# Kernel tuning notes

Measured on AMD Instinct MI355X. Metric: run time of the kernel, lower is better.

## Reference

```python
import jax, jax.numpy as jnp
import numpy as np
from jax.scipy.linalg import solve_triangular

CHUNK = 32


def _l2norm(x):
    return x / jnp.sqrt(jnp.sum(x * x, axis=-1, keepdims=True))


def setup_inputs() -> dict:
    key = jax.random.key(0)
    kq, kk, kv, kb = jax.random.split(key, 4)
    b, h, L, d = 2, 8, 4096, 128
    q = jax.random.normal(kq, (b, h, L, d), dtype=jnp.float32)
    k = jax.random.normal(kk, (b, h, L, d), dtype=jnp.float32)
    v = jax.random.normal(kv, (b, h, L, d), dtype=jnp.float32)
    beta = jax.random.uniform(kb, (b, h, L), dtype=jnp.float32)
    return {"q": q, "k": k, "v": v, "beta": beta}


def _delta_rule_chunkwise(q, k, v, beta, chunk_size=CHUNK):
    b, h, L, d_k = q.shape
    d_v = v.shape[-1]
    pad_len = (-L) % chunk_size
    if pad_len:
        q = jnp.pad(q, ((0, 0), (0, 0), (0, pad_len), (0, 0)))
        k = jnp.pad(k, ((0, 0), (0, 0), (0, pad_len), (0, 0)))
        v = jnp.pad(v, ((0, 0), (0, 0), (0, pad_len), (0, 0)))
        beta = jnp.pad(beta, ((0, 0), (0, 0), (0, pad_len)))
    L_pad = L + pad_len
    n = L_pad // chunk_size
    c = chunk_size

    q = _l2norm(q)
    k = _l2norm(k)
    v = v * beta[..., None]
    k_beta = k * beta[..., None]

    # -> [b, h, n, c, d]
    qc = q.reshape(b, h, n, c, d_k)
    kc = k.reshape(b, h, n, c, d_k)
    vc = v.reshape(b, h, n, c, d_v)
    kbc = k_beta.reshape(b, h, n, c, d_k)

    # Intra-chunk UT transform: inv = (I + strictly_lower(k_beta @ k^T))^{-1}
    # (equivalent to the sequential forward-substitution loop in the torch code)
    A = jnp.einsum('bhnce,bhnfe->bhncf', kbc, kc)          # [b,h,n,c,c]
    strict_lower = jnp.tril(jnp.ones((c, c), dtype=A.dtype), k=-1)
    T = A * strict_lower + jnp.eye(c, dtype=A.dtype)        # unit lower-triangular
    eye_b = jnp.broadcast_to(jnp.eye(c, dtype=A.dtype), T.shape)
    inv = solve_triangular(T, eye_b, lower=True)            # [b,h,n,c,c]

    u = jnp.einsum('bhncf,bhnfd->bhncd', inv, vc)           # [b,h,n,c,d_v]
    w = jnp.einsum('bhncf,bhnfk->bhnck', inv, kbc)          # [b,h,n,c,d_k]

    # Cross-chunk recurrence over n chunks (sequential in n)
    causal = jnp.tril(jnp.ones((c, c), dtype=q.dtype))      # incl. diagonal
    qs = jnp.moveaxis(qc, 2, 0)   # [n,b,h,c,d_k]
    ks = jnp.moveaxis(kc, 2, 0)
    us = jnp.moveaxis(u, 2, 0)
    ws = jnp.moveaxis(w, 2, 0)

    S0 = jnp.zeros((b, h, d_k, d_v), dtype=q.dtype)

    def step(S, xs):
        q_i, k_i, u_i, w_i = xs
        local_attn = jnp.einsum('bhce,bhfe->bhcf', q_i, k_i) * causal
        u_adj = u_i - jnp.einsum('bhck,bhkd->bhcd', w_i, S)
        o_i = jnp.einsum('bhck,bhkd->bhcd', q_i, S) \
            + jnp.einsum('bhcf,bhfd->bhcd', local_attn, u_adj)
        S_new = S + jnp.einsum('bhck,bhcd->bhkd', k_i, u_adj)
        return S_new, o_i

    S_final, outs = jax.lax.scan(step, S0, (qs, ks, us, ws))
    out = jnp.moveaxis(outs, 0, 2).reshape(b, h, L_pad, d_v)
    if pad_len:
        out = out[:, :, :L]
    return out, S_final


def reference(q, k, v, beta):
    return _delta_rule_chunkwise(q, k, v, beta)
```

## Files before the change

kernel.cpp:

```cpp
#include <hip/hip_runtime.h>


#define Bb 2
#define Hh 8
#define Ll 4096
#define Dd 128
#define DP (Dd + 4)
#define Cc 32
#define CP2 33
#define NC (Ll / Cc)
#define BHn (Bb * Hh)

#define SLAB 30720

typedef float  f32x16 __attribute__((ext_vector_type(16)));
typedef short  bf16x8 __attribute__((ext_vector_type(8)));

#define WAITVM(N) asm volatile("s_waitcnt vmcnt(" #N ")" ::: "memory")

__device__ __forceinline__ short f2bf(float x) {
    union { float f; unsigned u; } a; a.f = x;
    const unsigned r = a.u + 0x7FFFu + ((a.u >> 16) & 1u);
    return (short)(r >> 16);
}

__device__ __forceinline__ float bf2f(short h) {
    union { unsigned u; float f; } t;
    t.u = ((unsigned)(unsigned short)h) << 16;
    return t.f;
}

__device__ __forceinline__ unsigned cvt_pk_bf16(float lo, float hi) {
    unsigned r;
    asm("v_cvt_pk_bf16_f32 %0, %1, %2" : "=v"(r) : "v"(lo), "v"(hi));
    return r;
}

__device__ __forceinline__ bf16x8 mk_bop(const f32x16& T, int m) {
    const int o = 8 * m;
    const unsigned a01 = cvt_pk_bf16(T[o + 0], T[o + 1]);
    const unsigned a23 = cvt_pk_bf16(T[o + 2], T[o + 3]);
    const unsigned b01 = cvt_pk_bf16(T[o + 4], T[o + 5]);
    const unsigned b23 = cvt_pk_bf16(T[o + 6], T[o + 7]);
    const auto r0 = __builtin_amdgcn_permlane32_swap(a01, b01, false, false);
    const auto r1 = __builtin_amdgcn_permlane32_swap(a23, b23, false, false);
    union { unsigned u[4]; bf16x8 v; } out;
    out.u[0] = r0[0]; out.u[1] = r1[0]; out.u[2] = r0[1]; out.u[3] = r1[1];
    return out.v;
}

__device__ __forceinline__ void gl_lds16(const void* gsrc, void* ldst) {
    __builtin_amdgcn_global_load_lds(
        (const __attribute__((address_space(1))) unsigned int*)gsrc,
        (__attribute__((address_space(3))) unsigned int*)ldst, 16, 0, 0);
}

__device__ __forceinline__ void split8(const float4& a, const float4& b,
                                       bf16x8& hi, bf16x8& lo) {
    const float x[8] = {a.x, a.y, a.z, a.w, b.x, b.y, b.z, b.w};
    #pragma unroll
    for (int j = 0; j < 8; ++j) {
        const short hs = f2bf(x[j]);
        hi[j] = hs;
        lo[j] = f2bf(x[j] - bf2f(hs));
    }
}

__device__ __forceinline__ void fma4(float4& acc, float s, const float4& x) {
    acc.x += s * x.x; acc.y += s * x.y; acc.z += s * x.z; acc.w += s * x.w;
}

template <bool QNB>
__global__ __launch_bounds__(256, 4) void prep_kernel(
    const float* __restrict__ q, const float* __restrict__ k,
    const float* __restrict__ v, const float* __restrict__ beta,
    float* __restrict__ wsU, float* __restrict__ wsNq,
    short* __restrict__ wsWb, short* __restrict__ wsKtb,
    short* __restrict__ wsAttnb, short* __restrict__ wsQnb)
{
    __shared__ float sK[Cc][DP];
    __shared__ float sA[Cc][CP2];
    __shared__ float sInv[Cc][CP2];
    __shared__ float sBeta[Cc], sNk[Cc], sNq[Cc];

    const int tid = threadIdx.x;
    const int blk = blockIdx.x;
    const int bh = blk / NC;
    const int ch = blk % NC;
    const size_t base = (size_t)(bh * Ll + ch * Cc) * Dd;

    for (int e = tid; e < Cc * Dd / 4; e += 256) {
        const int r = e >> 5, c4 = e & 31;
        ((float4*)&sK[r][0])[c4] = ((const float4*)(k + base))[e];
    }
    if (tid < Cc) sBeta[tid] = beta[bh * Ll + ch * Cc + tid];
    __syncthreads();

    {
        const int row = tid >> 2, part = tid & 3;
        float s = 0.f;
        if (row < Cc) {
            const float4* src = (const float4*)&sK[row][0];
            #pragma unroll
            for (int j = 0; j < 8; ++j) {
                const float4 t = src[part + j * 4];
                s += t.x * t.x + t.y * t.y + t.z * t.z + t.w * t.w;
            }
        } else {
            const float4* src =
                (const float4*)(q + base + (size_t)(row - Cc) * Dd);
            #pragma unroll
            for (int j = 0; j < 8; ++j) {
                const float4 t = src[part + j * 4];
                s += t.x * t.x + t.y * t.y + t.z * t.z + t.w * t.w;
            }
        }
        s += __shfl_xor(s, 1);
        s += __shfl_xor(s, 2);
        if (part == 0) {
            const float r = 1.0f / sqrtf(s);
            if (row < Cc) sNk[row] = r; else sNq[row - Cc] = r;
        }
    }
    __syncthreads();

    if (tid < Cc) wsNq[bh * Ll + ch * Cc + tid] = sNq[tid];

    for (int e = tid; e < Cc * Dd / 4; e += 256) {
        const int r = e >> 5, c4 = e & 31;
        float4 kk = ((float4*)&sK[r][0])[c4];
        const float nk = sNk[r];
        kk.x *= nk; kk.y *= nk; kk.z *= nk; kk.w *= nk;
        ((float4*)&sK[r][0])[c4] = kk;
    }
    __syncthreads();

    const int wid = tid >> 6;
    const int lc = tid & 31;
    const int lh = (tid >> 5) & 1;
    const size_t cbase = (size_t)blk * Cc * Dd;
    const size_t abase = (size_t)blk * Cc * Cc;

    if (wid == 0) {
        f32x16 D, D2;
        #pragma unroll
        for (int r = 0; r < 16; ++r) { D[r] = 0.f; D2[r] = 0.f; }
        #pragma unroll
        for (int ks = 0; ks < 8; ++ks) {
            const float4 a = ((const float4*)&sK[lc][0])[4 * ks + 2 * lh];
            const float4 b = ((const float4*)&sK[lc][0])[4 * ks + 2 * lh + 1];
            bf16x8 hi, lo;
            split8(a, b, hi, lo);
            D  = __builtin_amdgcn_mfma_f32_32x32x16_bf16(hi, hi, D,  0, 0, 0);
            D2 = __builtin_amdgcn_mfma_f32_32x32x16_bf16(hi, lo, D2, 0, 0, 0);
            D2 = __builtin_amdgcn_mfma_f32_32x32x16_bf16(lo, hi, D2, 0, 0, 0);
        }
        #pragma unroll
        for (int r = 0; r < 16; ++r) {
            const int row = (r & 3) + 8 * (r >> 2) + 4 * lh;
            sA[row][lc] = (D[r] + D2[r]) * sBeta[row];
        }
        asm volatile("s_waitcnt lgkmcnt(0)" ::: "memory");
        __builtin_amdgcn_sched_barrier(0);

        float inv[Cc];
        #pragma unroll
        for (int m = 0; m < Cc; ++m) inv[m] = (m == lc) ? 1.f : 0.f;
        #pragma unroll
        for (int i = 1; i < Cc; ++i) {
            float s = 0.f;
            #pragma unroll
            for (int m = 0; m < i; ++m) s += sA[i][m] * inv[m];
            inv[i] = (lc == i) ? 1.f : -s;
        }
        if (lh == 0) {
            #pragma unroll
            for (int m = 0; m < Cc; ++m) sInv[m][lc] = inv[m];
        }
    } else if (wid == 1) {
        const float nq = sNq[lc];
        const float* qrow = q + base + (size_t)lc * Dd;
        f32x16 D, D2;
        #pragma unroll
        for (int r = 0; r < 16; ++r) { D[r] = 0.f; D2[r] = 0.f; }
        #pragma unroll
        for (int ks = 0; ks < 8; ++ks) {
            float4 a = ((const float4*)qrow)[4 * ks + 2 * lh];
            float4 b = ((const float4*)qrow)[4 * ks + 2 * lh + 1];
            a.x *= nq; a.y *= nq; a.z *= nq; a.w *= nq;
            b.x *= nq; b.y *= nq; b.z *= nq; b.w *= nq;
            bf16x8 hiQ, loQ;
            split8(a, b, hiQ, loQ);
            if constexpr (QNB) {
                ((bf16x8*)(wsQnb + cbase))[(2 * ks + lh) * 32 + lc] = hiQ;
            }
            const float4 ka = ((const float4*)&sK[lc][0])[4 * ks + 2 * lh];
            const float4 kb2 = ((const float4*)&sK[lc][0])[4 * ks + 2 * lh + 1];
            bf16x8 hiK, loK;
            split8(ka, kb2, hiK, loK);
            D  = __builtin_amdgcn_mfma_f32_32x32x16_bf16(hiQ, hiK, D,  0, 0, 0);
            D2 = __builtin_amdgcn_mfma_f32_32x32x16_bf16(hiQ, loK, D2, 0, 0, 0);
            D2 = __builtin_amdgcn_mfma_f32_32x32x16_bf16(loQ, hiK, D2, 0, 0, 0);
        }
        #pragma unroll
        for (int r = 0; r < 16; ++r) {
            const int row = (r & 3) + 8 * (r >> 2) + 4 * lh;
            const float val = (lc <= row) ? (D[r] + D2[r]) : 0.f;
            wsAttnb[abase + ((lc >> 3) << 8) + (row << 3) + (lc & 7)] =
                f2bf(val);
        }
    } else {
        const int t = tid - 128;
        #pragma unroll
        for (int it = 0; it < 4; ++it) {
            const int g = t + it * 128;
            const int B = g >> 5, ddl = g & 31;
            const int dd = ((B >> 2) << 5) + ddl;
            const int cc0 = (B & 3) << 3;
            bf16x8 pk;
            #pragma unroll
            for (int j = 0; j < 8; ++j) pk[j] = f2bf(sK[cc0 + j][dd]);
            ((bf16x8*)(wsKtb + cbase))[g] = pk;
        }
    }
    __syncthreads();

    {
        const int c = tid >> 3, g = tid & 7, dd0 = g * 16;
        float4 u0{}, u1{}, u2{}, u3{}, w0{}, w1{}, w2{}, w3{};
        for (int f = 0; f <= c; ++f) {
            const float ivb = sInv[c][f] * sBeta[f];
            const float4* vr = (const float4*)(v + base + (size_t)f * Dd + dd0);
            const float4* kr = (const float4*)&sK[f][dd0];
            fma4(u0, ivb, vr[0]); fma4(u1, ivb, vr[1]);
            fma4(u2, ivb, vr[2]); fma4(u3, ivb, vr[3]);
            fma4(w0, ivb, kr[0]); fma4(w1, ivb, kr[1]);
            fma4(w2, ivb, kr[2]); fma4(w3, ivb, kr[3]);
        }
        const int rh = (c & 3) + ((c >> 3) << 2) + (((c >> 2) & 1) << 4);
        const float uu[16] = {u0.x, u0.y, u0.z, u0.w, u1.x, u1.y, u1.z, u1.w,
                              u2.x, u2.y, u2.z, u2.w, u3.x, u3.y, u3.z, u3.w};
        #pragma unroll
        for (int j = 0; j < 16; ++j) {
            const int dd = dd0 + j;
            wsU[cbase + ((dd >> 5) << 10) + (rh << 5) + (dd & 31)] = uu[j];
        }
        bf16x8 p0, p1;
        p0[0] = f2bf(-w0.x); p0[1] = f2bf(-w0.y); p0[2] = f2bf(-w0.z);
        p0[3] = f2bf(-w0.w); p0[4] = f2bf(-w1.x); p0[5] = f2bf(-w1.y);
        p0[6] = f2bf(-w1.z); p0[7] = f2bf(-w1.w);
        p1[0] = f2bf(-w2.x); p1[1] = f2bf(-w2.y); p1[2] = f2bf(-w2.z);
        p1[3] = f2bf(-w2.w); p1[4] = f2bf(-w3.x); p1[5] = f2bf(-w3.y);
        p1[6] = f2bf(-w3.z); p1[7] = f2bf(-w3.w);
        ((bf16x8*)(wsWb + cbase))[(2 * g) * 32 + c] = p0;
        ((bf16x8*)(wsWb + cbase))[(2 * g + 1) * 32 + c] = p1;
    }
}

template <bool QNB>
__device__ __forceinline__ void stage_slab(
    char* slab, int bh, int ch, int colBase, int lane,
    const short* __restrict__ wsWb, const short* __restrict__ wsKtb,
    const short* __restrict__ wsQnb, const short* __restrict__ wsAttnb,
    const float* __restrict__ wsU)
{
    const size_t cb = (size_t)(bh * NC + ch) * (Cc * Dd);
    const size_t ab = (size_t)(bh * NC + ch) * (Cc * Cc);
    const char* srcW = (const char*)(wsWb + cb);
    const char* srcK = (const char*)(wsKtb + cb);
    const char* srcA = (const char*)(wsAttnb + ab);
    const int l16 = lane * 16;
    #pragma unroll
    for (int g = 0; g < 8; ++g)
        gl_lds16(srcW + g * 1024 + l16, slab + g * 1024);
    #pragma unroll
    for (int g = 0; g < 8; ++g)
        gl_lds16(srcK + g * 1024 + l16, slab + 8192 + g * 1024);
    if constexpr (QNB) {
        const char* srcQ = (const char*)(wsQnb + cb);
        #pragma unroll
        for (int g = 0; g < 8; ++g)
            gl_lds16(srcQ + g * 1024 + l16, slab + 16384 + g * 1024);
    }
    #pragma unroll
    for (int g = 0; g < 2; ++g)
        gl_lds16(srcA + g * 1024 + l16, slab + 24576 + g * 1024);
    const float* srcU = wsU + cb + (colBase << 5);
    #pragma unroll
    for (int g = 0; g < 4; ++g)
        gl_lds16(srcU + g * 256 + lane * 4, slab + 26624 + g * 1024);
}

template <bool QNB>
__device__ __forceinline__ void compute_chunk(
    const char* slab, int bh, int ch, int colBase, int c, int h,
    const float* __restrict__ q, const float* __restrict__ wsNq,
    f32x16& S0, f32x16& S1, f32x16& S2, f32x16& S3, float* __restrict__ out)
{
    const bf16x8* Wf = (const bf16x8*)slab;
    const bf16x8* Kf = (const bf16x8*)(slab + 8192);
    const bf16x8* Qf = (const bf16x8*)(slab + 16384);
    const bf16x8* Af = (const bf16x8*)(slab + 24576);
    const float*  Uf = (const float*)(slab + 26624);

    bf16x8 qa[8];
    if constexpr (QNB) {
        #pragma unroll
        for (int ks = 0; ks < 8; ++ks) qa[ks] = Qf[(2 * ks + h) * 32 + c];
    } else {
        const size_t qb = (size_t)(bh * Ll + ch * Cc) * Dd;
        const float rq = wsNq[bh * Ll + ch * Cc + c];
        #pragma unroll
        for (int ks = 0; ks < 8; ++ks) {
            const float4 a = ((const float4*)(q + qb))[c * 32 + 4 * ks + 2 * h];
            const float4 b = ((const float4*)(q + qb))[c * 32 + 4 * ks + 2 * h + 1];
            union { unsigned u[4]; bf16x8 v; } t;
            t.u[0] = cvt_pk_bf16(a.x * rq, a.y * rq);
            t.u[1] = cvt_pk_bf16(a.z * rq, a.w * rq);
            t.u[2] = cvt_pk_bf16(b.x * rq, b.y * rq);
            t.u[3] = cvt_pk_bf16(b.z * rq, b.w * rq);
            qa[ks] = t.v;
        }
    }

    f32x16 Ua, Ub, O1, O2;
    #pragma unroll
    for (int r = 0; r < 16; ++r) {
        Ua[r] = Uf[(r + 16 * h) * 32 + c];
        Ub[r] = 0.f; O1[r] = 0.f; O2[r] = 0.f;
    }

    #pragma unroll
    for (int ks = 0; ks < 8; ++ks) {
        const f32x16& T = (ks < 2) ? S0 : (ks < 4) ? S1 : (ks < 6) ? S2 : S3;
        const bf16x8 sB = mk_bop(T, ks & 1);
        const bf16x8 wA = Wf[(2 * ks + h) * 32 + c];
        if (ks < 4)
            Ua = __builtin_amdgcn_mfma_f32_32x32x16_bf16(wA, sB, Ua, 0, 0, 0);
        else
            Ub = __builtin_amdgcn_mfma_f32_32x32x16_bf16(wA, sB, Ub, 0, 0, 0);
        if (ks & 1)
            O2 = __builtin_amdgcn_mfma_f32_32x32x16_bf16(qa[ks], sB, O2, 0, 0, 0);
        else
            O1 = __builtin_amdgcn_mfma_f32_32x32x16_bf16(qa[ks], sB, O1, 0, 0, 0);
    }

    f32x16 Us;
    #pragma unroll
    for (int r = 0; r < 16; ++r) Us[r] = Ua[r] + Ub[r];

    const bf16x8 uB0 = mk_bop(Us, 0);
    const bf16x8 uB1 = mk_bop(Us, 1);

    S0 = __builtin_amdgcn_mfma_f32_32x32x16_bf16(Kf[(0 + h) * 32 + c],  uB0, S0, 0, 0, 0);
    S0 = __builtin_amdgcn_mfma_f32_32x32x16_bf16(Kf[(2 + h) * 32 + c],  uB1, S0, 0, 0, 0);
    S1 = __builtin_amdgcn_mfma_f32_32x32x16_bf16(Kf[(4 + h) * 32 + c],  uB0, S1, 0, 0, 0);
    S1 = __builtin_amdgcn_mfma_f32_32x32x16_bf16(Kf[(6 + h) * 32 + c],  uB1, S1, 0, 0, 0);
    S2 = __builtin_amdgcn_mfma_f32_32x32x16_bf16(Kf[(8 + h) * 32 + c],  uB0, S2, 0, 0, 0);
    S2 = __builtin_amdgcn_mfma_f32_32x32x16_bf16(Kf[(10 + h) * 32 + c], uB1, S2, 0, 0, 0);
    S3 = __builtin_amdgcn_mfma_f32_32x32x16_bf16(Kf[(12 + h) * 32 + c], uB0, S3, 0, 0, 0);
    S3 = __builtin_amdgcn_mfma_f32_32x32x16_bf16(Kf[(14 + h) * 32 + c], uB1, S3, 0, 0, 0);

    O1 = __builtin_amdgcn_mfma_f32_32x32x16_bf16(Af[(0 + h) * 32 + c], uB0, O1, 0, 0, 0);
    O2 = __builtin_amdgcn_mfma_f32_32x32x16_bf16(Af[(2 + h) * 32 + c], uB1, O2, 0, 0, 0);

    const size_t qb = (size_t)(bh * Ll + ch * Cc) * Dd;
    #pragma unroll
    for (int r = 0; r < 16; ++r) {
        const int row = (r & 3) + 8 * (r >> 2) + 4 * h;
        out[qb + (size_t)row * Dd + colBase + c] = O1[r] + O2[r];
    }
}

template <bool QNB>
__device__ __forceinline__ void pcstep(
    int ch, char* cur, char* nxt, bool dostage, int wid,
    int bh, int colBase, int c, int h, int lane,
    const float* __restrict__ q, const float* __restrict__ wsNq,
    const short* __restrict__ wsWb, const short* __restrict__ wsKtb,
    const short* __restrict__ wsAttnb, const short* __restrict__ wsQnb,
    const float* __restrict__ wsU,
    f32x16& S0, f32x16& S1, f32x16& S2, f32x16& S3, float* __restrict__ out)
{
    if (wid == 0) {
        compute_chunk<QNB>(cur, bh, ch, colBase, c, h, q, wsNq,
                           S0, S1, S2, S3, out);
    } else {
        if (dostage) {
            stage_slab<QNB>(nxt, bh, ch + 2, colBase, lane,
                            wsWb, wsKtb, wsQnb, wsAttnb, wsU);
            if constexpr (QNB) WAITVM(30); else WAITVM(22);
        } else {
            WAITVM(0);
        }
    }
    __builtin_amdgcn_s_barrier();
}

template <bool QNB>
__global__ __launch_bounds__(128, 1) void scan_kernel(
    const float* __restrict__ q, const float* __restrict__ wsU,
    const short* __restrict__ wsWb, const short* __restrict__ wsKtb,
    const short* __restrict__ wsAttnb, const short* __restrict__ wsQnb,
    const float* __restrict__ wsNq, float* __restrict__ out)
{
    __shared__ __attribute__((aligned(16))) char sl0[SLAB];
    __shared__ __attribute__((aligned(16))) char sl1[SLAB];
    __shared__ __attribute__((aligned(16))) char sl2[SLAB];

    const int tid = threadIdx.x;
    const int wid = tid >> 6;
    const int lane = tid & 63;
    const int h = lane >> 5;
    const int c = lane & 31;
    const int bh = blockIdx.x;
    const int colBase = blockIdx.y * 32;

    f32x16 S0, S1, S2, S3;
    #pragma unroll
    for (int r = 0; r < 16; ++r) { S0[r]=0.f; S1[r]=0.f; S2[r]=0.f; S3[r]=0.f; }

    if (wid == 1) {
        stage_slab<QNB>(sl0, bh, 0, colBase, lane, wsWb, wsKtb, wsQnb,
                        wsAttnb, wsU);
        stage_slab<QNB>(sl1, bh, 1, colBase, lane, wsWb, wsKtb, wsQnb,
                        wsAttnb, wsU);
        if constexpr (QNB) WAITVM(30); else WAITVM(22);
    }
    __builtin_amdgcn_s_barrier();

    #pragma unroll 1
    for (int it = 0; it < 42; ++it) {
        const int ch = it * 3;
        pcstep<QNB>(ch + 0, sl0, sl2, true, wid, bh, colBase, c, h, lane,
                    q, wsNq, wsWb, wsKtb, wsAttnb, wsQnb, wsU,
                    S0, S1, S2, S3, out);
        pcstep<QNB>(ch + 1, sl1, sl0, true, wid, bh, colBase, c, h, lane,
                    q, wsNq, wsWb, wsKtb, wsAttnb, wsQnb, wsU,
                    S0, S1, S2, S3, out);
        pcstep<QNB>(ch + 2, sl2, sl1, true, wid, bh, colBase, c, h, lane,
                    q, wsNq, wsWb, wsKtb, wsAttnb, wsQnb, wsU,
                    S0, S1, S2, S3, out);
    }
    pcstep<QNB>(126, sl0, sl2, false, wid, bh, colBase, c, h, lane,
                q, wsNq, wsWb, wsKtb, wsAttnb, wsQnb, wsU, S0, S1, S2, S3, out);
    pcstep<QNB>(127, sl1, sl0, false, wid, bh, colBase, c, h, lane,
                q, wsNq, wsWb, wsKtb, wsAttnb, wsQnb, wsU, S0, S1, S2, S3, out);

    if (wid == 0) {
        const size_t soff = (size_t)Bb * Hh * Ll * Dd;
        #pragma unroll
        for (int t = 0; t < 4; ++t) {
            const f32x16& T = (t == 0) ? S0 : (t == 1) ? S1 : (t == 2) ? S2 : S3;
            #pragma unroll
            for (int r = 0; r < 16; ++r) {
                const int row = 32 * t + (r & 3) + 8 * (r >> 2) + 4 * h;
                out[soff + (size_t)bh * Dd * Dd + (size_t)row * Dd + colBase + c]
                    = T[r];
            }
        }
    }
}

extern "C" void kernel_launch(void* const* d_in, const int* in_sizes, int n_in,
                              void* d_out, int out_size, void* d_ws,
                              size_t ws_size, hipStream_t stream) {
    const float* q    = (const float*)d_in[0];
    const float* k    = (const float*)d_in[1];
    const float* v    = (const float*)d_in[2];
    const float* beta = (const float*)d_in[3];
    float* out = (float*)d_out;

    const size_t nQK = (size_t)BHn * Ll * Dd;
    float* wsU    = (float*)d_ws;
    float* wsNq   = wsU + nQK;
    short* wsWb   = (short*)(wsNq + (size_t)BHn * Ll);
    short* wsKtb  = wsWb + nQK;
    short* wsAttnb = wsKtb + nQK;
    short* wsQnb  = wsAttnb + (size_t)BHn * NC * Cc * Cc;
    const size_t need_qnb = (size_t)((char*)(wsQnb + nQK) - (char*)d_ws);

    if (ws_size >= need_qnb) {
        prep_kernel<true><<<dim3(BHn * NC), 256, 0, stream>>>(
            q, k, v, beta, wsU, wsNq, wsWb, wsKtb, wsAttnb, wsQnb);
        scan_kernel<true><<<dim3(BHn, 4), 128, 0, stream>>>(
            q, wsU, wsWb, wsKtb, wsAttnb, wsQnb, wsNq, out);
    } else {
        prep_kernel<false><<<dim3(BHn * NC), 256, 0, stream>>>(
            q, k, v, beta, wsU, wsNq, wsWb, wsKtb, wsAttnb, wsQnb);
        scan_kernel<false><<<dim3(BHn, 4), 128, 0, stream>>>(
            q, wsU, wsWb, wsKtb, wsAttnb, wsQnb, wsNq, out);
    }
}
```

Before: 316.5 us.

## Split per-chunk scan compute across two waves with LDS exchange of partials

The sequential scan step was done by a single compute wave while a second wave staged the next slabs. Now two compute waves each handle half of the K dimension of the state (S0/S1 versus S2/S3). They exchange partial U and O sums through small LDS buffers with an extra barrier per chunk, and a third wave takes over staging. The goal is to shorten the serial MFMA dependency chain per chunk. The cost is an additional barrier per chunk and LDS traffic on the critical path.

```diff
diff --git a/kernel.cpp b/kernel.cpp
--- a/kernel.cpp
+++ b/kernel.cpp
@@ -17,6 +17,7 @@
 typedef short  bf16x8 __attribute__((ext_vector_type(8)));
 
 #define WAITVM(N) asm volatile("s_waitcnt vmcnt(" #N ")" ::: "memory")
+#define WAITLGKM0 asm volatile("s_waitcnt lgkmcnt(0)" ::: "memory")
 
 __device__ __forceinline__ short f2bf(float x) {
     union { float f; unsigned u; } a; a.f = x;
@@ -292,87 +293,6 @@
 }
 
 template <bool QNB>
-__device__ __forceinline__ void compute_chunk(
-    const char* slab, int bh, int ch, int colBase, int c, int h,
-    const float* __restrict__ q, const float* __restrict__ wsNq,
-    f32x16& S0, f32x16& S1, f32x16& S2, f32x16& S3, float* __restrict__ out)
-{
-    const bf16x8* Wf = (const bf16x8*)slab;
-    const bf16x8* Kf = (const bf16x8*)(slab + 8192);
-    const bf16x8* Qf = (const bf16x8*)(slab + 16384);
-    const bf16x8* Af = (const bf16x8*)(slab + 24576);
-    const float*  Uf = (const float*)(slab + 26624);
-
-    bf16x8 qa[8];
-    if constexpr (QNB) {
-        #pragma unroll
-        for (int ks = 0; ks < 8; ++ks) qa[ks] = Qf[(2 * ks + h) * 32 + c];
-    } else {
-        const size_t qb = (size_t)(bh * Ll + ch * Cc) * Dd;
-        const float rq = wsNq[bh * Ll + ch * Cc + c];
-        #pragma unroll
-        for (int ks = 0; ks < 8; ++ks) {
-            const float4 a = ((const float4*)(q + qb))[c * 32 + 4 * ks + 2 * h];
-            const float4 b = ((const float4*)(q + qb))[c * 32 + 4 * ks + 2 * h + 1];
-            union { unsigned u[4]; bf16x8 v; } t;
-            t.u[0] = cvt_pk_bf16(a.x * rq, a.y * rq);
-            t.u[1] = cvt_pk_bf16(a.z * rq, a.w * rq);
-            t.u[2] = cvt_pk_bf16(b.x * rq, b.y * rq);
-            t.u[3] = cvt_pk_bf16(b.z * rq, b.w * rq);
-            qa[ks] = t.v;
-        }
-    }
-
-    f32x16 Ua, Ub, O1, O2;
-    #pragma unroll
-    for (int r = 0; r < 16; ++r) {
-        Ua[r] = Uf[(r + 16 * h) * 32 + c];
-        Ub[r] = 0.f; O1[r] = 0.f; O2[r] = 0.f;
-    }
-
-    #pragma unroll
-    for (int ks = 0; ks < 8; ++ks) {
-        const f32x16& T = (ks < 2) ? S0 : (ks < 4) ? S1 : (ks < 6) ? S2 : S3;
-        const bf16x8 sB = mk_bop(T, ks & 1);
-        const bf16x8 wA = Wf[(2 * ks + h) * 32 + c];
-        if (ks < 4)
-            Ua = __builtin_amdgcn_mfma_f32_32x32x16_bf16(wA, sB, Ua, 0, 0, 0);
-        else
-            Ub = __builtin_amdgcn_mfma_f32_32x32x16_bf16(wA, sB, Ub, 0, 0, 0);
-        if (ks & 1)
-            O2 = __builtin_amdgcn_mfma_f32_32x32x16_bf16(qa[ks], sB, O2, 0, 0, 0);
-        else
-            O1 = __builtin_amdgcn_mfma_f32_32x32x16_bf16(qa[ks], sB, O1, 0, 0, 0);
-    }
-
-    f32x16 Us;
-    #pragma unroll
-    for (int r = 0; r < 16; ++r) Us[r] = Ua[r] + Ub[r];
-
-    const bf16x8 uB0 = mk_bop(Us, 0);
-    const bf16x8 uB1 = mk_bop(Us, 1);
-
-    S0 = __builtin_amdgcn_mfma_f32_32x32x16_bf16(Kf[(0 + h) * 32 + c],  uB0, S0, 0, 0, 0);
-    S0 = __builtin_amdgcn_mfma_f32_32x32x16_bf16(Kf[(2 + h) * 32 + c],  uB1, S0, 0, 0, 0);
-    S1 = __builtin_amdgcn_mfma_f32_32x32x16_bf16(Kf[(4 + h) * 32 + c],  uB0, S1, 0, 0, 0);
-    S1 = __builtin_amdgcn_mfma_f32_32x32x16_bf16(Kf[(6 + h) * 32 + c],  uB1, S1, 0, 0, 0);
-    S2 = __builtin_amdgcn_mfma_f32_32x32x16_bf16(Kf[(8 + h) * 32 + c],  uB0, S2, 0, 0, 0);
-    S2 = __builtin_amdgcn_mfma_f32_32x32x16_bf16(Kf[(10 + h) * 32 + c], uB1, S2, 0, 0, 0);
-    S3 = __builtin_amdgcn_mfma_f32_32x32x16_bf16(Kf[(12 + h) * 32 + c], uB0, S3, 0, 0, 0);
-    S3 = __builtin_amdgcn_mfma_f32_32x32x16_bf16(Kf[(14 + h) * 32 + c], uB1, S3, 0, 0, 0);
-
-    O1 = __builtin_amdgcn_mfma_f32_32x32x16_bf16(Af[(0 + h) * 32 + c], uB0, O1, 0, 0, 0);
-    O2 = __builtin_amdgcn_mfma_f32_32x32x16_bf16(Af[(2 + h) * 32 + c], uB1, O2, 0, 0, 0);
-
-    const size_t qb = (size_t)(bh * Ll + ch * Cc) * Dd;
-    #pragma unroll
-    for (int r = 0; r < 16; ++r) {
-        const int row = (r & 3) + 8 * (r >> 2) + 4 * h;
-        out[qb + (size_t)row * Dd + colBase + c] = O1[r] + O2[r];
-    }
-}
-
-template <bool QNB>
 __device__ __forceinline__ void pcstep(
     int ch, char* cur, char* nxt, bool dostage, int wid,
     int bh, int colBase, int c, int h, int lane,
@@ -380,11 +300,150 @@
     const short* __restrict__ wsWb, const short* __restrict__ wsKtb,
     const short* __restrict__ wsAttnb, const short* __restrict__ wsQnb,
     const float* __restrict__ wsU,
+    float (*xUA)[65], float (*xUB)[65], float (*xO)[65],
     f32x16& S0, f32x16& S1, f32x16& S2, f32x16& S3, float* __restrict__ out)
 {
+    const bf16x8* Wf = (const bf16x8*)cur;
+    const bf16x8* Kf = (const bf16x8*)(cur + 8192);
+    const bf16x8* Qf = (const bf16x8*)(cur + 16384);
+    const bf16x8* Af = (const bf16x8*)(cur + 24576);
+    const float*  Uf = (const float*)(cur + 26624);
+
+    f32x16 Ukeep, Oc, Od;
+    bf16x8 K4[4], AT0, AT1;
+
     if (wid == 0) {
-        compute_chunk<QNB>(cur, bh, ch, colBase, c, h, q, wsNq,
-                           S0, S1, S2, S3, out);
+        bf16x8 W[4], QA[4];
+        f32x16 U0;
+        #pragma unroll
+        for (int i = 0; i < 4; ++i) W[i]  = Wf[(2 * i + h) * 32 + c];
+        #pragma unroll
+        for (int i = 0; i < 4; ++i) K4[i] = Kf[(2 * i + h) * 32 + c];
+        if constexpr (QNB) {
+            #pragma unroll
+            for (int i = 0; i < 4; ++i) QA[i] = Qf[(2 * i + h) * 32 + c];
+        } else {
+            const size_t qb = (size_t)(bh * Ll + ch * Cc) * Dd;
+            const float rq = wsNq[bh * Ll + ch * Cc + c];
+            #pragma unroll
+            for (int i = 0; i < 4; ++i) {
+                const float4 a = ((const float4*)(q + qb))[c * 32 + 4 * i + 2 * h];
+                const float4 b = ((const float4*)(q + qb))[c * 32 + 4 * i + 2 * h + 1];
+                union { unsigned u[4]; bf16x8 v; } t;
+                t.u[0] = cvt_pk_bf16(a.x * rq, a.y * rq);
+                t.u[1] = cvt_pk_bf16(a.z * rq, a.w * rq);
+                t.u[2] = cvt_pk_bf16(b.x * rq, b.y * rq);
+                t.u[3] = cvt_pk_bf16(b.z * rq, b.w * rq);
+                QA[i] = t.v;
+            }
+        }
+        #pragma unroll
+        for (int r = 0; r < 16; ++r) U0[r] = Uf[(r + 16 * h) * 32 + c];
+
+        const bf16x8 sB0 = mk_bop(S0, 0), sB1 = mk_bop(S0, 1);
+        const bf16x8 sB2 = mk_bop(S1, 0), sB3 = mk_bop(S1, 1);
+
+        f32x16 Ua = U0, Ub;
+        #pragma unroll
+        for (int r = 0; r < 16; ++r) { Ub[r] = 0.f; Oc[r] = 0.f; Od[r] = 0.f; }
+        Ua = __builtin_amdgcn_mfma_f32_32x32x16_bf16(W[0], sB0, Ua, 0, 0, 0);
+        Ub = __builtin_amdgcn_mfma_f32_32x32x16_bf16(W[2], sB2, Ub, 0, 0, 0);
+        Oc = __builtin_amdgcn_mfma_f32_32x32x16_bf16(QA[0], sB0, Oc, 0, 0, 0);
+        Od = __builtin_amdgcn_mfma_f32_32x32x16_bf16(QA[2], sB2, Od, 0, 0, 0);
+        Ua = __builtin_amdgcn_mfma_f32_32x32x16_bf16(W[1], sB1, Ua, 0, 0, 0);
+        Ub = __builtin_amdgcn_mfma_f32_32x32x16_bf16(W[3], sB3, Ub, 0, 0, 0);
+        Oc = __builtin_amdgcn_mfma_f32_32x32x16_bf16(QA[1], sB1, Oc, 0, 0, 0);
+        Od = __builtin_amdgcn_mfma_f32_32x32x16_bf16(QA[3], sB3, Od, 0, 0, 0);
+
+        #pragma unroll
+        for (int r = 0; r < 16; ++r) {
+            Ukeep[r] = Ua[r] + Ub[r];
+            xUA[r][lane] = Ukeep[r];
+            xO[r][lane] = Oc[r] + Od[r];
+        }
+        WAITLGKM0;
+    } else if (wid == 1) {
+        bf16x8 W[4], QA[4];
+        #pragma unroll
+        for (int i = 0; i < 4; ++i) W[i]  = Wf[(2 * (i + 4) + h) * 32 + c];
+        #pragma unroll
+        for (int i = 0; i < 4; ++i) K4[i] = Kf[(2 * (i + 4) + h) * 32 + c];
+        if constexpr (QNB) {
+            #pragma unroll
+            for (int i = 0; i < 4; ++i) QA[i] = Qf[(2 * (i + 4) + h) * 32 + c];
+        } else {
+            const size_t qb = (size_t)(bh * Ll + ch * Cc) * Dd;
+            const float rq = wsNq[bh * Ll + ch * Cc + c];
+            #pragma unroll
+            for (int i = 0; i < 4; ++i) {
+                const int ks = i + 4;
+                const float4 a = ((const float4*)(q + qb))[c * 32 + 4 * ks + 2 * h];
+                const float4 b = ((const float4*)(q + qb))[c * 32 + 4 * ks + 2 * h + 1];
+                union { unsigned u[4]; bf16x8 v; } t;
+                t.u[0] = cvt_pk_bf16(a.x * rq, a.y * rq);
+                t.u[1] = cvt_pk_bf16(a.z * rq, a.w * rq);
+                t.u[2] = cvt_pk_bf16(b.x * rq, b.y * rq);
+                t.u[3] = cvt_pk_bf16(b.z * rq, b.w * rq);
+                QA[i] = t.v;
+            }
+        }
+        AT0 = Af[(0 + h) * 32 + c];
+        AT1 = Af[(2 + h) * 32 + c];
+
+        const bf16x8 sB4 = mk_bop(S2, 0), sB5 = mk_bop(S2, 1);
+        const bf16x8 sB6 = mk_bop(S3, 0), sB7 = mk_bop(S3, 1);
+
+        f32x16 Ua, Ub;
+        #pragma unroll
+        for (int r = 0; r < 16; ++r) { Ua[r] = 0.f; Ub[r] = 0.f;
+                                       Oc[r] = 0.f; Od[r] = 0.f; }
+        Ua = __builtin_amdgcn_mfma_f32_32x32x16_bf16(W[0], sB4, Ua, 0, 0, 0);
+        Ub = __builtin_amdgcn_mfma_f32_32x32x16_bf16(W[2], sB6, Ub, 0, 0, 0);
+        Oc = __builtin_amdgcn_mfma_f32_32x32x16_bf16(QA[0], sB4, Oc, 0, 0, 0);
+        Od = __builtin_amdgcn_mfma_f32_32x32x16_bf16(QA[2], sB6, Od, 0, 0, 0);
+        Ua = __builtin_amdgcn_mfma_f32_32x32x16_bf16(W[1], sB5, Ua, 0, 0, 0);
+        Ub = __builtin_amdgcn_mfma_f32_32x32x16_bf16(W[3], sB7, Ub, 0, 0, 0);
+        Oc = __builtin_amdgcn_mfma_f32_32x32x16_bf16(QA[1], sB5, Oc, 0, 0, 0);
+        Od = __builtin_amdgcn_mfma_f32_32x32x16_bf16(QA[3], sB7, Od, 0, 0, 0);
+
+        #pragma unroll
+        for (int r = 0; r < 16; ++r) {
+            Ukeep[r] = Ua[r] + Ub[r];
+            xUB[r][lane] = Ukeep[r];
+        }
+        WAITLGKM0;
+    }
+    __builtin_amdgcn_s_barrier();
+
+    if (wid == 0) {
+        f32x16 Us;
+        #pragma unroll
+        for (int r = 0; r < 16; ++r) Us[r] = Ukeep[r] + xUB[r][lane];
+        const bf16x8 uB0 = mk_bop(Us, 0);
+        const bf16x8 uB1 = mk_bop(Us, 1);
+        S0 = __builtin_amdgcn_mfma_f32_32x32x16_bf16(K4[0], uB0, S0, 0, 0, 0);
+        S1 = __builtin_amdgcn_mfma_f32_32x32x16_bf16(K4[2], uB0, S1, 0, 0, 0);
+        S0 = __builtin_amdgcn_mfma_f32_32x32x16_bf16(K4[1], uB1, S0, 0, 0, 0);
+        S1 = __builtin_amdgcn_mfma_f32_32x32x16_bf16(K4[3], uB1, S1, 0, 0, 0);
+    } else if (wid == 1) {
+        f32x16 Us;
+        #pragma unroll
+        for (int r = 0; r < 16; ++r) Us[r] = Ukeep[r] + xUA[r][lane];
+        const bf16x8 uB0 = mk_bop(Us, 0);
+        const bf16x8 uB1 = mk_bop(Us, 1);
+        S2 = __builtin_amdgcn_mfma_f32_32x32x16_bf16(K4[0], uB0, S2, 0, 0, 0);
+        S3 = __builtin_amdgcn_mfma_f32_32x32x16_bf16(K4[2], uB0, S3, 0, 0, 0);
+        S2 = __builtin_amdgcn_mfma_f32_32x32x16_bf16(K4[1], uB1, S2, 0, 0, 0);
+        S3 = __builtin_amdgcn_mfma_f32_32x32x16_bf16(K4[3], uB1, S3, 0, 0, 0);
+        Oc = __builtin_amdgcn_mfma_f32_32x32x16_bf16(AT0, uB0, Oc, 0, 0, 0);
+        Od = __builtin_amdgcn_mfma_f32_32x32x16_bf16(AT1, uB1, Od, 0, 0, 0);
+        const size_t qb = (size_t)(bh * Ll + ch * Cc) * Dd;
+        #pragma unroll
+        for (int r = 0; r < 16; ++r) {
+            const int row = (r & 3) + 8 * (r >> 2) + 4 * h;
+            out[qb + (size_t)row * Dd + colBase + c] =
+                (Oc[r] + Od[r]) + xO[r][lane];
+        }
     } else {
         if (dostage) {
             stage_slab<QNB>(nxt, bh, ch + 2, colBase, lane,
@@ -398,7 +457,7 @@
 }
 
 template <bool QNB>
-__global__ __launch_bounds__(128, 1) void scan_kernel(
+__global__ __launch_bounds__(192, 1) void scan_kernel(
     const float* __restrict__ q, const float* __restrict__ wsU,
     const short* __restrict__ wsWb, const short* __restrict__ wsKtb,
     const short* __restrict__ wsAttnb, const short* __restrict__ wsQnb,
@@ -407,6 +466,7 @@
     __shared__ __attribute__((aligned(16))) char sl0[SLAB];
     __shared__ __attribute__((aligned(16))) char sl1[SLAB];
     __shared__ __attribute__((aligned(16))) char sl2[SLAB];
+    __shared__ float xUA[16][65], xUB[16][65], xO[16][65];
 
     const int tid = threadIdx.x;
     const int wid = tid >> 6;
@@ -420,7 +480,7 @@
     #pragma unroll
     for (int r = 0; r < 16; ++r) { S0[r]=0.f; S1[r]=0.f; S2[r]=0.f; S3[r]=0.f; }
 
-    if (wid == 1) {
+    if (wid == 2) {
         stage_slab<QNB>(sl0, bh, 0, colBase, lane, wsWb, wsKtb, wsQnb,
                         wsAttnb, wsU);
         stage_slab<QNB>(sl1, bh, 1, colBase, lane, wsWb, wsKtb, wsQnb,
@@ -434,24 +494,37 @@
         const int ch = it * 3;
         pcstep<QNB>(ch + 0, sl0, sl2, true, wid, bh, colBase, c, h, lane,
                     q, wsNq, wsWb, wsKtb, wsAttnb, wsQnb, wsU,
-                    S0, S1, S2, S3, out);
+                    xUA, xUB, xO, S0, S1, S2, S3, out);
         pcstep<QNB>(ch + 1, sl1, sl0, true, wid, bh, colBase, c, h, lane,
                     q, wsNq, wsWb, wsKtb, wsAttnb, wsQnb, wsU,
-                    S0, S1, S2, S3, out);
+                    xUA, xUB, xO, S0, S1, S2, S3, out);
         pcstep<QNB>(ch + 2, sl2, sl1, true, wid, bh, colBase, c, h, lane,
                     q, wsNq, wsWb, wsKtb, wsAttnb, wsQnb, wsU,
-                    S0, S1, S2, S3, out);
+                    xUA, xUB, xO, S0, S1, S2, S3, out);
     }
     pcstep<QNB>(126, sl0, sl2, false, wid, bh, colBase, c, h, lane,
-                q, wsNq, wsWb, wsKtb, wsAttnb, wsQnb, wsU, S0, S1, S2, S3, out);
+                q, wsNq, wsWb, wsKtb, wsAttnb, wsQnb, wsU,
+                xUA, xUB, xO, S0, S1, S2, S3, out);
     pcstep<QNB>(127, sl1, sl0, false, wid, bh, colBase, c, h, lane,
-                q, wsNq, wsWb, wsKtb, wsAttnb, wsQnb, wsU, S0, S1, S2, S3, out);
-
+                q, wsNq, wsWb, wsKtb, wsAttnb, wsQnb, wsU,
+                xUA, xUB, xO, S0, S1, S2, S3, out);
+
+    const size_t soff = (size_t)Bb * Hh * Ll * Dd;
     if (wid == 0) {
-        const size_t soff = (size_t)Bb * Hh * Ll * Dd;
-        #pragma unroll
-        for (int t = 0; t < 4; ++t) {
-            const f32x16& T = (t == 0) ? S0 : (t == 1) ? S1 : (t == 2) ? S2 : S3;
+        #pragma unroll
+        for (int t = 0; t < 2; ++t) {
+            const f32x16& T = (t == 0) ? S0 : S1;
+            #pragma unroll
+            for (int r = 0; r < 16; ++r) {
+                const int row = 32 * t + (r & 3) + 8 * (r >> 2) + 4 * h;
+                out[soff + (size_t)bh * Dd * Dd + (size_t)row * Dd + colBase + c]
+                    = T[r];
+            }
+        }
+    } else if (wid == 1) {
+        #pragma unroll
+        for (int t = 2; t < 4; ++t) {
+            const f32x16& T = (t == 2) ? S2 : S3;
             #pragma unroll
             for (int r = 0; r < 16; ++r) {
                 const int row = 32 * t + (r & 3) + 8 * (r >> 2) + 4 * h;
@@ -483,12 +556,12 @@
     if (ws_size >= need_qnb) {
         prep_kernel<true><<<dim3(BHn * NC), 256, 0, stream>>>(
             q, k, v, beta, wsU, wsNq, wsWb, wsKtb, wsAttnb, wsQnb);
-        scan_kernel<true><<<dim3(BHn, 4), 128, 0, stream>>>(
+        scan_kernel<true><<<dim3(BHn, 4), 192, 0, stream>>>(
             q, wsU, wsWb, wsKtb, wsAttnb, wsQnb, wsNq, out);
     } else {
         prep_kernel<false><<<dim3(BHn * NC), 256, 0, stream>>>(
             q, k, v, beta, wsU, wsNq, wsWb, wsKtb, wsAttnb, wsQnb);
-        scan_kernel<false><<<dim3(BHn, 4), 128, 0, stream>>>(
+        scan_kernel<false><<<dim3(BHn, 4), 192, 0, stream>>>(
             q, wsU, wsWb, wsKtb, wsAttnb, wsQnb, wsNq, out);
     }
 }
```

Measured after the change: 377.5 us. 19.3% more time.
